# Performance work log

Hardware: AMD Instinct MI355X
Metric: run time of the kernel (lower is better)

## Reference

```python
import jax, jax.numpy as jnp
import numpy as np

DIM_GATE = 256
DIM_BIAS = 128
H = 8
D = 32
EPS = 1e-5


def _layernorm(t, gamma, beta):
    mu = jnp.mean(t, axis=-1, keepdims=True)
    var = jnp.mean(jnp.square(t - mu), axis=-1, keepdims=True)
    return (t - mu) * jax.lax.rsqrt(var + EPS) * gamma + beta


def setup_inputs() -> dict:
    key = jax.random.key(0)
    ks = jax.random.split(key, 12)
    b, l = 2, 512
    x = jax.random.normal(ks[0], (b, l, DIM_GATE), dtype=jnp.float32)
    bias = jax.random.normal(ks[1], (b, l, l, DIM_BIAS), dtype=jnp.float32)
    s_g = 1.0 / np.sqrt(DIM_GATE)
    s_b = 1.0 / np.sqrt(DIM_BIAS)
    return {
        "x": x,
        "bias": bias,
        "g_gamma": jnp.ones((DIM_GATE,), jnp.float32),
        "g_beta": jnp.zeros((DIM_GATE,), jnp.float32),
        "b_gamma": jnp.ones((DIM_BIAS,), jnp.float32),
        "b_beta": jnp.zeros((DIM_BIAS,), jnp.float32),
        "Wq": jax.random.normal(ks[2], (DIM_GATE, H * D), jnp.float32) * s_g,
        "Wk": jax.random.normal(ks[3], (DIM_GATE, H * D), jnp.float32) * s_g,
        "Wv": jax.random.normal(ks[4], (DIM_GATE, H * D), jnp.float32) * s_g,
        "Wb": jax.random.normal(ks[5], (DIM_BIAS, H), jnp.float32) * s_b,
        "Wg": jax.random.normal(ks[6], (DIM_GATE, H * D), jnp.float32) * s_g,
        "bg": jnp.zeros((H * D,), jnp.float32),
        "Wout": jax.random.normal(ks[7], (H * D, DIM_GATE), jnp.float32) * s_g,
        "bout": jnp.zeros((DIM_GATE,), jnp.float32),
    }


def reference(x, bias, g_gamma, g_beta, b_gamma, b_beta, Wq, Wk, Wv, Wb, Wg, bg, Wout, bout):
    b, l, _ = x.shape
    scaling = 1.0 / np.sqrt(D)
    xn = _layernorm(x, g_gamma, g_beta)                      # [b,l,dg]
    bn = _layernorm(bias, b_gamma, b_beta)                   # [b,l,l,db]
    q = (xn @ Wq).reshape(b, l, H, D)                        # [b,l,h,d]
    k = (xn @ Wk).reshape(b, l, H, D) * scaling
    v = (xn @ Wv).reshape(b, l, H, D)
    pair_b = bn @ Wb                                         # [b,q,k,h]
    gate = jax.nn.sigmoid(xn @ Wg + bg)                      # [b,l,h*d]
    attn = jnp.einsum('bqhd,bkhd->bqkh', q, k) + pair_b      # [b,q,k,h]
    attn = jax.nn.softmax(attn, axis=-2)                     # softmax over k
    out = jnp.einsum('bqkh,bkhd->bqhd', attn, v).reshape(b, l, H * D)
    out = gate * out
    return out @ Wout + bout
```

## Files before the change

kernel.cpp:

```cpp
#include <hip/hip_runtime.h>
#include <math.h>

#define LSEQ 512
#define DG 256
#define DB 128
#define NH 8
#define HD 32
#define EPSV 1e-5f
#define LP2 516

typedef __attribute__((ext_vector_type(8))) short bf16x8;
typedef __attribute__((ext_vector_type(4))) float f32x4;

__device__ __forceinline__ unsigned short f2bf(float x) {
    unsigned int u = __float_as_uint(x);
    u += 0x7FFFu + ((u >> 16) & 1u);
    return (unsigned short)(u >> 16);
}
__device__ __forceinline__ float bf2f(unsigned short h) {
    return __uint_as_float(((unsigned int)h) << 16);
}

__global__ __launch_bounds__(256) void prep_kernel(
    const float* __restrict__ x, const float* __restrict__ g_gamma,
    const float* __restrict__ g_beta, const float* __restrict__ Wq,
    const float* __restrict__ Wk, const float* __restrict__ Wv,
    const float* __restrict__ Wg, const float* __restrict__ bg,
    float* __restrict__ q_ws, float* __restrict__ k_ws,
    float* __restrict__ v_ws, float* __restrict__ g_ws)
{
    __shared__ float xs[4][DG];
    const int t = threadIdx.x;
    const int wave = t >> 6, lane = t & 63;
    const int row0 = blockIdx.x << 2;

    {
        const int row = row0 + wave;
        const float4 xv = *(const float4*)(x + (size_t)row * DG + lane * 4);
        float s  = xv.x + xv.y + xv.z + xv.w;
        float ss = xv.x*xv.x + xv.y*xv.y + xv.z*xv.z + xv.w*xv.w;
        #pragma unroll
        for (int m = 32; m >= 1; m >>= 1) { s += __shfl_xor(s, m); ss += __shfl_xor(ss, m); }
        const float mean = s * (1.f / DG);
        const float rstd = rsqrtf(ss * (1.f / DG) - mean * mean + EPSV);
        const float4 gg = *(const float4*)(g_gamma + lane * 4);
        const float4 gb = *(const float4*)(g_beta + lane * 4);
        float4 xo;
        xo.x = (xv.x - mean) * rstd * gg.x + gb.x;
        xo.y = (xv.y - mean) * rstd * gg.y + gb.y;
        xo.z = (xv.z - mean) * rstd * gg.z + gb.z;
        xo.w = (xv.w - mean) * rstd * gg.w + gb.w;
        *(float4*)&xs[wave][lane * 4] = xo;
    }
    __syncthreads();

    float aq[4] = {0,0,0,0}, ak[4] = {0,0,0,0}, av[4] = {0,0,0,0}, ag[4] = {0,0,0,0};
    #pragma unroll 4
    for (int c = 0; c < DG; ++c) {
        const float wq = Wq[(size_t)c * DG + t];
        const float wk = Wk[(size_t)c * DG + t];
        const float wv = Wv[(size_t)c * DG + t];
        const float wg = Wg[(size_t)c * DG + t];
        #pragma unroll
        for (int r = 0; r < 4; ++r) {
            const float xr = xs[r][c];
            aq[r] = fmaf(xr, wq, aq[r]);
            ak[r] = fmaf(xr, wk, ak[r]);
            av[r] = fmaf(xr, wv, av[r]);
            ag[r] = fmaf(xr, wg, ag[r]);
        }
    }

    const float scal = 0.17677669529663687f;
    const float bgv = bg[t];
    #pragma unroll
    for (int r = 0; r < 4; ++r) {
        const size_t o = (size_t)(row0 + r) * DG + t;
        q_ws[o] = aq[r];
        k_ws[o] = ak[r] * scal;
        v_ws[o] = av[r];
        g_ws[o] = 1.f / (1.f + __expf(-(ag[r] + bgv)));
    }
}

__global__ __launch_bounds__(256) void pairb_kernel(
    const float* __restrict__ bias, const float* __restrict__ b_gamma,
    const float* __restrict__ b_beta, const float* __restrict__ Wb,
    float* __restrict__ pair_ws)
{
    __shared__ float lds[4 * 2 * 2048];
    const int t = threadIdx.x;
    const int w = t >> 6, l = t & 63;
    const int n = l & 15, quad = l >> 4;
    const int bq = blockIdx.x;

    bf16x8 gwhi[4], gwlo[4];
    float S1 = 0.f, S0 = 0.f;
    #pragma unroll
    for (int ks = 0; ks < 4; ++ks) {
        #pragma unroll
        for (int j = 0; j < 8; ++j) {
            const int c = ks * 32 + quad * 8 + j;
            const float wb = (n < 8) ? Wb[c * 8 + n] : 0.f;
            const float wv = b_gamma[c] * wb;
            S1 += wv;
            S0 += b_beta[c] * wb;
            unsigned short hi = f2bf(wv);
            unsigned short lo = f2bf(wv - bf2f(hi));
            if (n == 8) { hi = 0x3F80; lo = 0; }
            gwhi[ks][j] = (short)hi;
            gwlo[ks][j] = (short)lo;
        }
    }
    S1 += __shfl_xor(S1, 16); S1 += __shfl_xor(S1, 32);
    S0 += __shfl_xor(S0, 16); S0 += __shfl_xor(S0, 32);

    float* myl = lds + w * 4096;
    const size_t rowbase = (size_t)bq * LSEQ + w * 16;

    auto stage = [&](int tt, int buf) {
        const float* src = bias + (rowbase + (size_t)tt * 64) * DB;
        float* dst = myl + buf * 2048;
        #pragma unroll
        for (int i = 0; i < 8; ++i) {
            __builtin_amdgcn_global_load_lds(
                (const __attribute__((address_space(1))) void*)(src + i * 256 + l * 4),
                (__attribute__((address_space(3))) void*)(dst + i * 256 + l * 4),
                16, 0, 0);
        }
    };

    auto compute = [&](int tt, int buf) {
        const float* d = myl + buf * 2048 + n * 128 + quad * 8;
        f32x4 acc = {0.f, 0.f, 0.f, 0.f};
        float ssq = 0.f;
        #pragma unroll
        for (int ks = 0; ks < 4; ++ks) {
            const float4 x0 = *(const float4*)(d + ks * 32);
            const float4 x1 = *(const float4*)(d + ks * 32 + 4);
            ssq = fmaf(x0.x,x0.x, fmaf(x0.y,x0.y, fmaf(x0.z,x0.z, fmaf(x0.w,x0.w, ssq))));
            ssq = fmaf(x1.x,x1.x, fmaf(x1.y,x1.y, fmaf(x1.z,x1.z, fmaf(x1.w,x1.w, ssq))));
            const float xsv[8] = {x0.x,x0.y,x0.z,x0.w,x1.x,x1.y,x1.z,x1.w};
            bf16x8 ahi, alo;
            #pragma unroll
            for (int j = 0; j < 8; ++j) {
                const unsigned short hi = f2bf(xsv[j]);
                ahi[j] = (short)hi;
                alo[j] = (short)f2bf(xsv[j] - bf2f(hi));
            }
            acc = __builtin_amdgcn_mfma_f32_16x16x32_bf16(ahi, gwhi[ks], acc, 0, 0, 0);
            acc = __builtin_amdgcn_mfma_f32_16x16x32_bf16(alo, gwhi[ks], acc, 0, 0, 0);
            acc = __builtin_amdgcn_mfma_f32_16x16x32_bf16(ahi, gwlo[ks], acc, 0, 0, 0);
        }
        ssq += __shfl_xor(ssq, 16);
        ssq += __shfl_xor(ssq, 32);
        float* pout = pair_ws + (rowbase + (size_t)tt * 64 + quad * 4) * NH + n;
        #pragma unroll
        for (int reg = 0; reg < 4; ++reg) {
            const float sumr = __uint_as_float((unsigned)__builtin_amdgcn_ds_bpermute(
                (quad * 16 + 8) * 4, (int)__float_as_uint(acc[reg])));
            const float ssqr = __uint_as_float((unsigned)__builtin_amdgcn_ds_bpermute(
                (quad * 4 + reg) * 4, (int)__float_as_uint(ssq)));
            const float mean = sumr * (1.f / DB);
            const float var  = ssqr * (1.f / DB) - mean * mean;
            const float rstd = rsqrtf(var + EPSV);
            const float p = rstd * (acc[reg] - mean * S1) + S0;
            if (n < NH) pout[reg * NH] = p;
        }
    };

    stage(0, 0);
    stage(1, 1);
    asm volatile("s_waitcnt vmcnt(8)" ::: "memory");
    compute(0, 0);
    for (int tt = 1; tt < 7; ++tt) {
        stage(tt + 1, (tt + 1) & 1);
        asm volatile("s_waitcnt vmcnt(12)" ::: "memory");
        compute(tt, tt & 1);
    }
    asm volatile("s_waitcnt vmcnt(4)" ::: "memory");
    compute(7, 1);
}

__global__ __launch_bounds__(512) void attn_kernel(
    const float* __restrict__ pair_ws, const float* __restrict__ Wout,
    const float* __restrict__ bout, const float* __restrict__ q_ws,
    const float* __restrict__ k_ws, const float* __restrict__ v_ws,
    const float* __restrict__ g_ws, float* __restrict__ out)
{
    __shared__ float lg[2 * NH * LP2];
    __shared__ float q_s[2 * DG];
    __shared__ float ps[4 * 2 * 64 * 4];
    __shared__ float row_s[2 * DG];
    __shared__ float rden[16];

    const int t = threadIdx.x;
    const int b = blockIdx.x >> 8;
    const int q0 = (blockIdx.x & 255) * 2;

    {
        const float* pbase = pair_ws + ((size_t)(b * LSEQ + q0)) * LSEQ * NH;
        #pragma unroll
        for (int r = 0; r < 4; ++r) {
            const int f = r * 512 + t;
            const float4 pv = *(const float4*)(pbase + (size_t)f * 4);
            const int q = f >> 10;
            const int o = (f * 4) & 4095;
            const int k = o >> 3, hb = o & 7;
            float* dst = lg + (q * NH + hb) * LP2 + k;
            dst[0] = pv.x; dst[LP2] = pv.y; dst[2*LP2] = pv.z; dst[3*LP2] = pv.w;
        }
        q_s[t] = q_ws[((size_t)(b * LSEQ + q0)) * DG + t];
    }
    __syncthreads();

    {
        const int h = t >> 6, kk = t & 63;
        const float* kb = k_ws + ((size_t)(b * LSEQ)) * DG + h * HD;
        const float* qp0 = q_s + h * HD;
        const float* qp1 = q_s + DG + h * HD;
        for (int j = 0; j < 8; ++j) {
            const int k = kk + j * 64;
            const float* kr = kb + (size_t)k * DG;
            float a0 = 0.f, a1 = 0.f;
            #pragma unroll
            for (int c = 0; c < 8; ++c) {
                const float4 kv = *(const float4*)(kr + c * 4);
                const float4 qa = *(const float4*)(qp0 + c * 4);
                const float4 qb = *(const float4*)(qp1 + c * 4);
                a0 = fmaf(kv.x, qa.x, fmaf(kv.y, qa.y, fmaf(kv.z, qa.z, fmaf(kv.w, qa.w, a0))));
                a1 = fmaf(kv.x, qb.x, fmaf(kv.y, qb.y, fmaf(kv.z, qb.z, fmaf(kv.w, qb.w, a1))));
            }
            lg[(0 * NH + h) * LP2 + k] += a0;
            lg[(1 * NH + h) * LP2 + k] += a1;
        }
    }
    __syncthreads();

    {
        const int qh = t >> 5, l32 = t & 31;
        float* lrow = lg + qh * LP2;
        float mx = -1e30f;
        #pragma unroll
        for (int i = 0; i < 16; ++i) mx = fmaxf(mx, lrow[l32 + i * 32]);
        #pragma unroll
        for (int m = 16; m >= 1; m >>= 1) mx = fmaxf(mx, __shfl_xor(mx, m));
        float s = 0.f;
        #pragma unroll
        for (int i = 0; i < 16; ++i) {
            const int k = l32 + i * 32;
            const float e = __expf(lrow[k] - mx);
            lrow[k] = e;
            s += e;
        }
        #pragma unroll
        for (int m = 16; m >= 1; m >>= 1) s += __shfl_xor(s, m);
        if (l32 == 0) rden[qh] = 1.f / s;
    }
    __syncthreads();

    {
        const int q = t >> 8, s4 = (t >> 6) & 3, c4 = t & 63;
        const int h = c4 >> 3;
        const float* vb = v_ws + ((size_t)(b * LSEQ + s4 * 128)) * DG + c4 * 4;
        const float* prow = lg + (q * NH + h) * LP2 + s4 * 128;
        float4 a = {0.f, 0.f, 0.f, 0.f};
        #pragma unroll 4
        for (int i = 0; i < 128; ++i) {
            const float p = prow[i];
            const float4 vv = *(const float4*)(vb + (size_t)i * DG);
            a.x = fmaf(p, vv.x, a.x);
            a.y = fmaf(p, vv.y, a.y);
            a.z = fmaf(p, vv.z, a.z);
            a.w = fmaf(p, vv.w, a.w);
        }
        *(float4*)&ps[((s4 * 2 + q) * 64 + c4) * 4] = a;
    }
    __syncthreads();
    if (t < 128) {
        const int q = t >> 6, c4 = t & 63, h = c4 >> 3;
        float4 a = *(const float4*)&ps[((0 * 2 + q) * 64 + c4) * 4];
        #pragma unroll
        for (int s4 = 1; s4 < 4; ++s4) {
            const float4 p4 = *(const float4*)&ps[((s4 * 2 + q) * 64 + c4) * 4];
            a.x += p4.x; a.y += p4.y; a.z += p4.z; a.w += p4.w;
        }
        const float sc = rden[q * NH + h];
        const float4 g4 = *(const float4*)(g_ws + ((size_t)(b * LSEQ + q0 + q)) * DG + c4 * 4);
        float* rs = row_s + q * DG + c4 * 4;
        rs[0] = a.x * sc * g4.x;
        rs[1] = a.y * sc * g4.y;
        rs[2] = a.z * sc * g4.z;
        rs[3] = a.w * sc * g4.w;
    }
    __syncthreads();

    {
        const int q = t >> 8, co = t & 255;
        const float* rs = row_s + q * DG;
        const float* wo = Wout + co;
        float a = 0.f;
        #pragma unroll 4
        for (int c = 0; c < DG; ++c)
            a = fmaf(rs[c], wo[(size_t)c * DG], a);
        out[((size_t)(b * LSEQ + q0 + q)) * DG + co] = a + bout[co];
    }
}

extern "C" void kernel_launch(void* const* d_in, const int* in_sizes, int n_in,
                              void* d_out, int out_size, void* d_ws, size_t ws_size,
                              hipStream_t stream)
{
    const float* x       = (const float*)d_in[0];
    const float* bias    = (const float*)d_in[1];
    const float* g_gamma = (const float*)d_in[2];
    const float* g_beta  = (const float*)d_in[3];
    const float* b_gamma = (const float*)d_in[4];
    const float* b_beta  = (const float*)d_in[5];
    const float* Wq      = (const float*)d_in[6];
    const float* Wk      = (const float*)d_in[7];
    const float* Wv      = (const float*)d_in[8];
    const float* Wb      = (const float*)d_in[9];
    const float* Wg      = (const float*)d_in[10];
    const float* bg      = (const float*)d_in[11];
    const float* Wout    = (const float*)d_in[12];
    const float* bout    = (const float*)d_in[13];
    float* out = (float*)d_out;

    float* ws      = (float*)d_ws;
    float* q_ws    = ws;
    float* k_ws    = ws + 262144;
    float* v_ws    = ws + 2 * 262144;
    float* g_ws    = ws + 3 * 262144;
    float* pair_ws = ws + 4 * 262144;

    hipLaunchKernelGGL(prep_kernel, dim3(256), dim3(256), 0, stream,
                       x, g_gamma, g_beta, Wq, Wk, Wv, Wg, bg,
                       q_ws, k_ws, v_ws, g_ws);
    hipLaunchKernelGGL(pairb_kernel, dim3(1024), dim3(256), 0, stream,
                       bias, b_gamma, b_beta, Wb, pair_ws);
    hipLaunchKernelGGL(attn_kernel, dim3(512), dim3(512), 0, stream,
                       pair_ws, Wout, bout, q_ws, k_ws, v_ws, g_ws, out);
}
```

Baseline: 536.5 us.

## Merge prep and pair-bias kernels into one launch; restructure QK logits loop

Fuses the LayerNorm/QKVG projection kernel and the pair-bias kernel into a single grid, with the first 256 blocks doing prep and the rest doing pair-bias, reusing the shared buffer. This removes one launch and lets the two independent stages run concurrently on the GPU. Separately, the QK logit computation in the attention kernel is reorganised so that 8 lanes each load a float4 slice of a K row, giving coalesced K reads, and partial dot products are combined with cross-lane shuffles. The shuffle reduction adds instructions, and only one lane in eight performs the LDS update.

After: 473.3 us. 1.13x faster.

```diff
diff --git a/kernel.cpp b/kernel.cpp
--- a/kernel.cpp
+++ b/kernel.cpp
@@ -21,78 +21,78 @@
     return __uint_as_float(((unsigned int)h) << 16);
 }
 
-__global__ __launch_bounds__(256) void prep_kernel(
+__global__ __launch_bounds__(256) void prep_pairb_kernel(
     const float* __restrict__ x, const float* __restrict__ g_gamma,
     const float* __restrict__ g_beta, const float* __restrict__ Wq,
     const float* __restrict__ Wk, const float* __restrict__ Wv,
     const float* __restrict__ Wg, const float* __restrict__ bg,
     float* __restrict__ q_ws, float* __restrict__ k_ws,
-    float* __restrict__ v_ws, float* __restrict__ g_ws)
-{
-    __shared__ float xs[4][DG];
-    const int t = threadIdx.x;
-    const int wave = t >> 6, lane = t & 63;
-    const int row0 = blockIdx.x << 2;
-
-    {
-        const int row = row0 + wave;
-        const float4 xv = *(const float4*)(x + (size_t)row * DG + lane * 4);
-        float s  = xv.x + xv.y + xv.z + xv.w;
-        float ss = xv.x*xv.x + xv.y*xv.y + xv.z*xv.z + xv.w*xv.w;
-        #pragma unroll
-        for (int m = 32; m >= 1; m >>= 1) { s += __shfl_xor(s, m); ss += __shfl_xor(ss, m); }
-        const float mean = s * (1.f / DG);
-        const float rstd = rsqrtf(ss * (1.f / DG) - mean * mean + EPSV);
-        const float4 gg = *(const float4*)(g_gamma + lane * 4);
-        const float4 gb = *(const float4*)(g_beta + lane * 4);
-        float4 xo;
-        xo.x = (xv.x - mean) * rstd * gg.x + gb.x;
-        xo.y = (xv.y - mean) * rstd * gg.y + gb.y;
-        xo.z = (xv.z - mean) * rstd * gg.z + gb.z;
-        xo.w = (xv.w - mean) * rstd * gg.w + gb.w;
-        *(float4*)&xs[wave][lane * 4] = xo;
-    }
-    __syncthreads();
-
-    float aq[4] = {0,0,0,0}, ak[4] = {0,0,0,0}, av[4] = {0,0,0,0}, ag[4] = {0,0,0,0};
-    #pragma unroll 4
-    for (int c = 0; c < DG; ++c) {
-        const float wq = Wq[(size_t)c * DG + t];
-        const float wk = Wk[(size_t)c * DG + t];
-        const float wv = Wv[(size_t)c * DG + t];
-        const float wg = Wg[(size_t)c * DG + t];
-        #pragma unroll
-        for (int r = 0; r < 4; ++r) {
-            const float xr = xs[r][c];
-            aq[r] = fmaf(xr, wq, aq[r]);
-            ak[r] = fmaf(xr, wk, ak[r]);
-            av[r] = fmaf(xr, wv, av[r]);
-            ag[r] = fmaf(xr, wg, ag[r]);
-        }
-    }
-
-    const float scal = 0.17677669529663687f;
-    const float bgv = bg[t];
-    #pragma unroll
-    for (int r = 0; r < 4; ++r) {
-        const size_t o = (size_t)(row0 + r) * DG + t;
-        q_ws[o] = aq[r];
-        k_ws[o] = ak[r] * scal;
-        v_ws[o] = av[r];
-        g_ws[o] = 1.f / (1.f + __expf(-(ag[r] + bgv)));
-    }
-}
-
-__global__ __launch_bounds__(256) void pairb_kernel(
+    float* __restrict__ v_ws, float* __restrict__ g_ws,
     const float* __restrict__ bias, const float* __restrict__ b_gamma,
     const float* __restrict__ b_beta, const float* __restrict__ Wb,
     float* __restrict__ pair_ws)
 {
     __shared__ float lds[4 * 2 * 2048];
     const int t = threadIdx.x;
+
+    if (blockIdx.x < 256) {
+        float (*xs)[DG] = (float(*)[DG])lds;
+        const int wave = t >> 6, lane = t & 63;
+        const int row0 = blockIdx.x << 2;
+
+        {
+            const int row = row0 + wave;
+            const float4 xv = *(const float4*)(x + (size_t)row * DG + lane * 4);
+            float s  = xv.x + xv.y + xv.z + xv.w;
+            float ss = xv.x*xv.x + xv.y*xv.y + xv.z*xv.z + xv.w*xv.w;
+            #pragma unroll
+            for (int m = 32; m >= 1; m >>= 1) { s += __shfl_xor(s, m); ss += __shfl_xor(ss, m); }
+            const float mean = s * (1.f / DG);
+            const float rstd = rsqrtf(ss * (1.f / DG) - mean * mean + EPSV);
+            const float4 gg = *(const float4*)(g_gamma + lane * 4);
+            const float4 gb = *(const float4*)(g_beta + lane * 4);
+            float4 xo;
+            xo.x = (xv.x - mean) * rstd * gg.x + gb.x;
+            xo.y = (xv.y - mean) * rstd * gg.y + gb.y;
+            xo.z = (xv.z - mean) * rstd * gg.z + gb.z;
+            xo.w = (xv.w - mean) * rstd * gg.w + gb.w;
+            *(float4*)&xs[wave][lane * 4] = xo;
+        }
+        __syncthreads();
+
+        float aq[4] = {0,0,0,0}, ak[4] = {0,0,0,0}, av[4] = {0,0,0,0}, ag[4] = {0,0,0,0};
+        #pragma unroll 4
+        for (int c = 0; c < DG; ++c) {
+            const float wq = Wq[(size_t)c * DG + t];
+            const float wk = Wk[(size_t)c * DG + t];
+            const float wv = Wv[(size_t)c * DG + t];
+            const float wg = Wg[(size_t)c * DG + t];
+            #pragma unroll
+            for (int r = 0; r < 4; ++r) {
+                const float xr = xs[r][c];
+                aq[r] = fmaf(xr, wq, aq[r]);
+                ak[r] = fmaf(xr, wk, ak[r]);
+                av[r] = fmaf(xr, wv, av[r]);
+                ag[r] = fmaf(xr, wg, ag[r]);
+            }
+        }
+
+        const float scal = 0.17677669529663687f;
+        const float bgv = bg[t];
+        #pragma unroll
+        for (int r = 0; r < 4; ++r) {
+            const size_t o = (size_t)(row0 + r) * DG + t;
+            q_ws[o] = aq[r];
+            k_ws[o] = ak[r] * scal;
+            v_ws[o] = av[r];
+            g_ws[o] = 1.f / (1.f + __expf(-(ag[r] + bgv)));
+        }
+        return;
+    }
+
     const int w = t >> 6, l = t & 63;
     const int n = l & 15, quad = l >> 4;
-    const int bq = blockIdx.x;
+    const int bq = blockIdx.x - 256;
 
     bf16x8 gwhi[4], gwlo[4];
     float S1 = 0.f, S0 = 0.f;
@@ -215,24 +215,24 @@
     __syncthreads();
 
     {
-        const int h = t >> 6, kk = t & 63;
-        const float* kb = k_ws + ((size_t)(b * LSEQ)) * DG + h * HD;
-        const float* qp0 = q_s + h * HD;
-        const float* qp1 = q_s + DG + h * HD;
-        for (int j = 0; j < 8; ++j) {
-            const int k = kk + j * 64;
-            const float* kr = kb + (size_t)k * DG;
-            float a0 = 0.f, a1 = 0.f;
-            #pragma unroll
-            for (int c = 0; c < 8; ++c) {
-                const float4 kv = *(const float4*)(kr + c * 4);
-                const float4 qa = *(const float4*)(qp0 + c * 4);
-                const float4 qb = *(const float4*)(qp1 + c * 4);
-                a0 = fmaf(kv.x, qa.x, fmaf(kv.y, qa.y, fmaf(kv.z, qa.z, fmaf(kv.w, qa.w, a0))));
-                a1 = fmaf(kv.x, qb.x, fmaf(kv.y, qb.y, fmaf(kv.z, qb.z, fmaf(kv.w, qb.w, a1))));
-            }
-            lg[(0 * NH + h) * LP2 + k] += a0;
-            lg[(1 * NH + h) * LP2 + k] += a1;
+        const int h = t >> 6;
+        const int lane = t & 63;
+        const int d4 = lane >> 3, r = lane & 7;
+        const float4 qa = *(const float4*)(q_s + h * HD + d4 * 4);
+        const float4 qb = *(const float4*)(q_s + DG + h * HD + d4 * 4);
+        const float* kbase = k_ws + ((size_t)(b * LSEQ)) * DG + h * HD + d4 * 4;
+        float* l0 = lg + (0 * NH + h) * LP2;
+        float* l1 = lg + (1 * NH + h) * LP2;
+        #pragma unroll 4
+        for (int kb8 = 0; kb8 < 64; ++kb8) {
+            const int krow = kb8 * 8 + r;
+            const float4 kv = *(const float4*)(kbase + (size_t)krow * DG);
+            float a0 = fmaf(kv.x, qa.x, fmaf(kv.y, qa.y, fmaf(kv.z, qa.z, kv.w * qa.w)));
+            float a1 = fmaf(kv.x, qb.x, fmaf(kv.y, qb.y, fmaf(kv.z, qb.z, kv.w * qb.w)));
+            a0 += __shfl_xor(a0, 8);  a1 += __shfl_xor(a1, 8);
+            a0 += __shfl_xor(a0, 16); a1 += __shfl_xor(a1, 16);
+            a0 += __shfl_xor(a0, 32); a1 += __shfl_xor(a1, 32);
+            if (d4 == 0) { l0[krow] += a0; l1[krow] += a1; }
         }
     }
     __syncthreads();
@@ -334,10 +334,9 @@
     float* g_ws    = ws + 3 * 262144;
     float* pair_ws = ws + 4 * 262144;
 
-    hipLaunchKernelGGL(prep_kernel, dim3(256), dim3(256), 0, stream,
+    hipLaunchKernelGGL(prep_pairb_kernel, dim3(1280), dim3(256), 0, stream,
                        x, g_gamma, g_beta, Wq, Wk, Wv, Wg, bg,
-                       q_ws, k_ws, v_ws, g_ws);
-    hipLaunchKernelGGL(pairb_kernel, dim3(1024), dim3(256), 0, stream,
+                       q_ws, k_ws, v_ws, g_ws,
                        bias, b_gamma, b_beta, Wb, pair_ws);
     hipLaunchKernelGGL(attn_kernel, dim3(512), dim3(512), 0, stream,
                        pair_ws, Wout, bout, q_ws, k_ws, v_ws, g_ws, out);
```
